# Kernel tuning notes

Hardware: AMD Instinct MI355X
Metric: run time of the kernel (lower is better)

Reference implementation:

```python
import math
import jax, jax.numpy as jnp
import numpy as np

# Model dims (from Weatherformer defaults: hidden = 8 heads * factor 8 = 64)
B, S, E, H, L = 8, 1024, 64, 8, 3
HD = E // H          # head_dim = 8
FF = 4 * E           # feedforward = 256
IN = 31              # input_dim (weather features)
OUT = 31             # output_dim
NG = 31              # granularity embedding table size
EPS = 1e-5


def setup_inputs() -> dict:
    key = jax.random.key(0)
    ks = jax.random.split(key, 12)
    p = lambda k, shape: jax.random.normal(k, shape, jnp.float32) * 0.05
    return {
        "weather": jax.random.normal(ks[0], (B, S, IN), jnp.float32),
        "coords": jax.random.uniform(ks[1], (B, 2), jnp.float32, -90.0, 90.0),
        "temporal_index": jax.random.randint(ks[2], (B, 2), 0, NG),
        "W_emb": p(ks[3], (IN, E)), "b_emb": jnp.zeros((E,), jnp.float32),
        "W_qkv": p(ks[4], (L, E, 3 * E)), "b_qkv": jnp.zeros((L, 3 * E), jnp.float32),
        "W_out": p(ks[5], (L, E, E)), "b_out": jnp.zeros((L, E), jnp.float32),
        "gran": p(ks[6], (L, NG, E)),
        "g1": jnp.ones((L, E), jnp.float32), "be1": jnp.zeros((L, E), jnp.float32),
        "W1": p(ks[7], (L, E, FF)), "b1": jnp.zeros((L, FF), jnp.float32),
        "W2": p(ks[8], (L, FF, E)), "b2": jnp.zeros((L, E), jnp.float32),
        "g2": jnp.ones((L, E), jnp.float32), "be2": jnp.zeros((L, E), jnp.float32),
        "W_fc": p(ks[9], (E, OUT)), "b_fc": jnp.zeros((OUT,), jnp.float32),
    }


def _layernorm(x, g, b):
    m = jnp.mean(x, axis=-1, keepdims=True)
    v = jnp.var(x, axis=-1, keepdims=True)
    return (x - m) / jnp.sqrt(v + EPS) * g + b


def _pos_encoding(coords):
    # div_term over every 4th channel: [E/4]
    div = jnp.exp(jnp.arange(0, E, 4, dtype=jnp.float32) * (-math.log(10000.0) / E))
    lat = coords[:, :1] / 180.0 * math.pi   # [B,1]
    lon = coords[:, 1:] / 180.0 * math.pi   # [B,1]
    tf = jnp.arange(S, dtype=jnp.float32)[:, None] * div          # [S, E/4]
    q = E // 4
    sin_tf = jnp.broadcast_to(jnp.sin(tf)[None], (B, S, q))       # channels 0::4
    cos_tf = jnp.broadcast_to(jnp.cos(tf)[None], (B, S, q))       # channels 1::4
    sin_lat = jnp.broadcast_to(jnp.sin(lat * div)[:, None, :], (B, S, q))  # 2::4
    cos_lon = jnp.broadcast_to(jnp.cos(lon * div)[:, None, :], (B, S, q))  # 3::4
    return jnp.stack([sin_tf, cos_tf, sin_lat, cos_lon], axis=-1).reshape(B, S, E)


def _attention(x, tg, W_qkv, b_qkv, W_out, b_out, gran_table):
    # Faithful replication of torch's (seq-major) qkv reshape quirk.
    qkv = x @ W_qkv + b_qkv                                  # [B,S,3E]
    qkv = qkv.reshape(B, S, 3, E).transpose(2, 0, 1, 3)      # [3,B,S,E]
    qkv = qkv.reshape(3, S, B * H, HD).transpose(0, 2, 1, 3) # [3,B*H,S,HD]
    q, k, v = qkv[0], qkv[1], qkv[2]
    ge = gran_table[tg].reshape(B * H, 1, HD)                # [B*H,1,HD]
    q = q + ge
    k = k + ge
    scores = jnp.einsum('bqd,bkd->bqk', q, k) * (HD ** -0.5) # [B*H,S,S]
    w = jax.nn.softmax(scores, axis=-1)                      # dropout = identity (eval)
    o = jnp.einsum('bqk,bkd->bqd', w, v)                     # [B*H,S,HD]
    o = o.transpose(1, 0, 2).reshape(B * S, E)
    return (o @ W_out + b_out).reshape(B, S, E)


def reference(weather, coords, temporal_index, W_emb, b_emb, W_qkv, b_qkv,
              W_out, b_out, gran, g1, be1, W1, b1, W2, b2, g2, be2, W_fc, b_fc):
    tg = temporal_index[:, 1:][:, :, None].astype(jnp.int32)  # [B,1,1]
    x = weather @ W_emb + b_emb                               # [B,S,E]
    x = x + _pos_encoding(coords)
    for l in range(L):
        a = _attention(x, tg, W_qkv[l], b_qkv[l], W_out[l], b_out[l], gran[l])
        x = _layernorm(x + a, g1[l], be1[l])
        ff = jax.nn.relu(x @ W1[l] + b1[l]) @ W2[l] + b2[l]
        x = _layernorm(x + ff, g2[l], be2[l])
    return x @ W_fc + b_fc                                    # [B,S,OUT]
```

## Files before the change

kernel.cpp:

```cpp
#include <hip/hip_runtime.h>
#include <math.h>

#define EPS 1e-5f

typedef float f32x16 __attribute__((ext_vector_type(16)));
typedef short short8 __attribute__((ext_vector_type(8)));

union U4S8 { uint4 u; short8 s; };

__device__ __forceinline__ float wave_sum64(float v) {
#pragma unroll
  for (int off = 32; off >= 1; off >>= 1) v += __shfl_xor(v, off, 64);
  return v;
}

__device__ __forceinline__ unsigned int bf16rne(float f) {
  unsigned int u = __float_as_uint(f);
  return (u + 0x7fffu + ((u >> 16) & 1u)) >> 16;
}
__device__ __forceinline__ float blo(unsigned int u) {
  return __uint_as_float(u << 16);
}
__device__ __forceinline__ float bhi(unsigned int u) {
  return __uint_as_float(u & 0xffff0000u);
}
__device__ __forceinline__ unsigned int cvt_pk_bf16(float lo, float hi) {
  unsigned int r;
  asm("v_cvt_pk_bf16_f32 %0, %1, %2" : "=v"(r) : "v"(lo), "v"(hi));
  return r;
}

__global__ __launch_bounds__(256) void k_prep(
    const float* __restrict__ Wo, const float* __restrict__ W1,
    const float* __restrict__ W2, const float* __restrict__ Wq,
    unsigned int* __restrict__ wbo, unsigned int* __restrict__ w1b,
    unsigned int* __restrict__ w2b, unsigned int* __restrict__ wqb) {
  int i = blockIdx.x * 256 + threadIdx.x;
  if (i < 6144) {
    int l = i >> 11, rem = i & 2047, p = rem >> 6, c = rem & 63;
    const float* s = Wo + l * 4096;
    wbo[i] = bf16rne(s[(2 * p) * 64 + c]) | (bf16rne(s[(2 * p + 1) * 64 + c]) << 16);
  }
  {
    int l = i / 8192, rem = i & 8191, p = rem >> 8, c = rem & 255;
    const float* s = W1 + (size_t)l * 16384;
    w1b[i] = bf16rne(s[(2 * p) * 256 + c]) | (bf16rne(s[(2 * p + 1) * 256 + c]) << 16);
  }
  {
    int l = i / 8192, rem = i & 8191, p = rem >> 6, c = rem & 63;
    const float* s = W2 + (size_t)l * 16384;
    w2b[i] = bf16rne(s[(2 * p) * 64 + c]) | (bf16rne(s[(2 * p + 1) * 64 + c]) << 16);
  }
  if (i < 12288) {
    int l = i / 6144, rem = i % 6144, p = rem / 192, c = rem % 192;
    const float* s = Wq + (size_t)(l + 1) * 12288;
    wqb[i] = bf16rne(s[(2 * p) * 192 + c]) | (bf16rne(s[(2 * p + 1) * 192 + c]) << 16);
  }
}

__global__ __launch_bounds__(192) void k_qkv0(
    const float* __restrict__ weather, const float* __restrict__ coords,
    const float* __restrict__ W_emb, const float* __restrict__ b_emb,
    const float* __restrict__ Wq, const float* __restrict__ bq,
    const float* __restrict__ gran, const int* __restrict__ tidx,
    float* __restrict__ x, unsigned int* __restrict__ qb,
    unsigned int* __restrict__ kbuf, unsigned short* __restrict__ vt) {
  int t = threadIdx.x;
  int row0 = blockIdx.x << 3;
  __shared__ float wrow[8][32];
  __shared__ float xs[8][64];
  for (int i = t; i < 256; i += 192) {
    int r = i >> 5, c2 = i & 31;
    if (c2 < 31) wrow[r][c2] = weather[(size_t)(row0 + r) * 31 + c2];
  }
  __syncthreads();
  int b = row0 >> 10;
  float lat = coords[b * 2 + 0] * 0.017453292519943295f;
  float lon = coords[b * 2 + 1] * 0.017453292519943295f;
  for (int idx = t; idx < 512; idx += 192) {
    int r = idx >> 6, e = idx & 63;
    int s = (row0 + r) & 1023;
    float acc = b_emb[e];
#pragma unroll
    for (int i = 0; i < 31; ++i) acc = fmaf(wrow[r][i], W_emb[i * 64 + e], acc);
    int g = e >> 2, rem = e & 3;
    float div = __expf(-0.5756462732485115f * (float)g);
    float pe;
    if (rem == 0)      pe = sinf((float)s * div);
    else if (rem == 1) pe = cosf((float)s * div);
    else if (rem == 2) pe = sinf(lat * div);
    else               pe = cosf(lon * div);
    float xv = acc + pe;
    xs[r][e] = xv;
    x[(size_t)(row0 + r) * 64 + e] = xv;
  }
  __syncthreads();
  float acc[8];
  float bias = bq[t];
#pragma unroll
  for (int r = 0; r < 8; ++r) acc[r] = bias;
#pragma unroll 4
  for (int k4 = 0; k4 < 16; ++k4) {
    float4 xv[8];
#pragma unroll
    for (int r = 0; r < 8; ++r) xv[r] = *(const float4*)(&xs[r][4 * k4]);
    float w0 = Wq[(4 * k4 + 0) * 192 + t];
    float w1 = Wq[(4 * k4 + 1) * 192 + t];
    float w2 = Wq[(4 * k4 + 2) * 192 + t];
    float w3 = Wq[(4 * k4 + 3) * 192 + t];
#pragma unroll
    for (int r = 0; r < 8; ++r) {
      acc[r] = fmaf(xv[r].x, w0, acc[r]);
      acc[r] = fmaf(xv[r].y, w1, acc[r]);
      acc[r] = fmaf(xv[r].z, w2, acc[r]);
      acc[r] = fmaf(xv[r].w, w3, acc[r]);
    }
  }
  int cq = t & 63;
  int hh = cq >> 3, hd = t & 7;
  int shi = (row0 & 1023) >> 3;
  int s2 = (b << 7) | shi;
  const float scl = 0.35355339059327373f;
#pragma unroll
  for (int r = 0; r < 8; ++r) {
    float o = acc[r];
    if (t < 128) o += gran[tidx[2 * r + 1] * 64 + cq];
    int bh = (r << 3) | hh;
    if (t < 64) {
      o *= scl;
      float nb = __shfl_down(o, 1, 64);
      if ((hd & 1) == 0)
        qb[((((size_t)bh << 10) | s2) << 2) + (hd >> 1)] =
            bf16rne(o) | (bf16rne(nb) << 16);
    } else if (t < 128) {
      float nb = __shfl_down(o, 1, 64);
      if ((hd & 1) == 0)
        kbuf[((((size_t)bh << 10) | s2) << 2) + (hd >> 1)] =
            bf16rne(o) | (bf16rne(nb) << 16);
    } else {
      vt[((size_t)bh << 13) + (hd << 10) + s2] = (unsigned short)bf16rne(o);
    }
  }
}

__global__ __launch_bounds__(512, 2) void k_attn(
    const unsigned int* __restrict__ qb, const unsigned int* __restrict__ kbuf,
    const unsigned short* __restrict__ vt, float* __restrict__ ao) {
  int bh = blockIdx.x >> 3, chunk = blockIdx.x & 7;
  int slo = bh >> 3, h = bh & 7;
  int t = threadIdx.x;
  int l = t & 63, w = t >> 6;
  int grp = w >> 1, kh = w & 1;
  int lq = l & 31, g = l >> 5;
  bool kl = (l < 32);
  bool vl = (lq < 8);
  int q = (chunk << 7) + (grp << 5) + lq;

  U4S8 qf;
  qf.u = make_uint4(0, 0, 0, 0);
  if (kl) qf.u = *(const uint4*)(qb + ((((size_t)bh << 10) + q) << 2));

  const uint4* kp = (const uint4*)(kbuf + ((size_t)bh << 12));
  const unsigned short* vp = vt + ((size_t)bh << 13);

  f32x16 O, Z;
#pragma unroll
  for (int i = 0; i < 16; ++i) { O[i] = 0.f; Z[i] = 0.f; }
  float m = -1e30f, ls = 0.f;

  int kb0 = kh << 4;
  for (int kblk = kb0; kblk < kb0 + 16; ++kblk) {
    U4S8 af;
    af.u = make_uint4(0, 0, 0, 0);
    if (kl) af.u = kp[(kblk << 5) + lq];
    f32x16 S = __builtin_amdgcn_mfma_f32_32x32x16_bf16(af.s, qf.s, Z, 0, 0, 0);

    float mx = S[0];
#pragma unroll
    for (int i = 1; i < 16; ++i) mx = fmaxf(mx, S[i]);
    mx = fmaxf(mx, __shfl_xor(mx, 32, 64));
    if (mx > m + 8.f) {
      float esc = __expf(m - mx);
      ls *= esc;
      O *= esc;
      m = mx;
    }
    float p[16];
#pragma unroll
    for (int i = 0; i < 16; ++i) p[i] = __expf(S[i] - m);
    float s01 = (p[0] + p[1]) + (p[2] + p[3]);
    float s23 = (p[4] + p[5]) + (p[6] + p[7]);
    float s45 = (p[8] + p[9]) + (p[10] + p[11]);
    float s67 = (p[12] + p[13]) + (p[14] + p[15]);
    ls += (s01 + s23) + (s45 + s67);

    unsigned va = cvt_pk_bf16(p[0], p[1]),  vb = cvt_pk_bf16(p[2], p[3]);
    unsigned vc = cvt_pk_bf16(p[4], p[5]),  vd = cvt_pk_bf16(p[6], p[7]);
    unsigned ve = cvt_pk_bf16(p[8], p[9]),  vf = cvt_pk_bf16(p[10], p[11]);
    unsigned vg = cvt_pk_bf16(p[12], p[13]), vh = cvt_pk_bf16(p[14], p[15]);
    unsigned sa = __shfl_xor((int)va, 32, 64), sb = __shfl_xor((int)vb, 32, 64);
    unsigned sc = __shfl_xor((int)vc, 32, 64), sd = __shfl_xor((int)vd, 32, 64);
    unsigned se = __shfl_xor((int)ve, 32, 64), sf = __shfl_xor((int)vf, 32, 64);
    unsigned sg = __shfl_xor((int)vg, 32, 64), sh = __shfl_xor((int)vh, 32, 64);
    U4S8 b1, b2;
    b1.u.x = kl ? va : sc;  b1.u.y = kl ? vb : sd;
    b1.u.z = kl ? sa : vc;  b1.u.w = kl ? sb : vd;
    b2.u.x = kl ? ve : sg;  b2.u.y = kl ? vf : sh;
    b2.u.z = kl ? se : vg;  b2.u.w = kl ? sf : vh;

    U4S8 v1, v2;
    v1.u = make_uint4(0, 0, 0, 0);
    v2.u = make_uint4(0, 0, 0, 0);
    if (vl) {
      const unsigned short* vb8 = vp + (lq << 10) + (kblk << 5) + (g << 3);
      v1.u = *(const uint4*)vb8;
      v2.u = *(const uint4*)(vb8 + 16);
    }
    O = __builtin_amdgcn_mfma_f32_32x32x16_bf16(v1.s, b1.s, O, 0, 0, 0);
    O = __builtin_amdgcn_mfma_f32_32x32x16_bf16(v2.s, b2.s, O, 0, 0, 0);
  }

  ls += __shfl_xor(ls, 32, 64);

  __shared__ float pm[4][64], pl[4][64];
  __shared__ float po[4][64][4];
  if (kh == 0) {
    pm[grp][l] = m;
    pl[grp][l] = ls;
    *(float4*)(&po[grp][l][0]) = make_float4(O[0], O[1], O[2], O[3]);
  }
  __syncthreads();
  if (kh == 1) {
    float mA = pm[grp][l], lsA = pl[grp][l];
    float nm = fmaxf(m, mA);
    float wB = __expf(m - nm), wA = __expf(mA - nm);
    float4 oA = *(const float4*)(&po[grp][l][0]);
    float inv = 1.0f / (ls * wB + lsA * wA);
    int bq2 = q >> 7, sq = ((q & 127) << 3) | slo;
    float* op = ao + (((size_t)((bq2 << 10) | sq)) << 6) + (h << 3) + (g << 2);
    *(float4*)op = make_float4((O[0] * wB + oA.x * wA) * inv,
                               (O[1] * wB + oA.y * wA) * inv,
                               (O[2] * wB + oA.z * wA) * inv,
                               (O[3] * wB + oA.w * wA) * inv);
  }
}

template <bool EMIT, bool HEAD>
__global__ __launch_bounds__(256, 4) void k_fused(
    const float* x_in, const float* __restrict__ ao,
    const unsigned int* __restrict__ Wo, const float* __restrict__ bo,
    const float* __restrict__ g1, const float* __restrict__ be1,
    const unsigned int* __restrict__ W1, const float* __restrict__ b1,
    const unsigned int* __restrict__ W2, const float* __restrict__ b2,
    const float* __restrict__ g2, const float* __restrict__ be2,
    const unsigned int* __restrict__ Wq, const float* __restrict__ bq,
    const float* __restrict__ gran, const int* __restrict__ tidx,
    unsigned int* __restrict__ qbo, unsigned int* __restrict__ kbo,
    unsigned short* __restrict__ vto,
    const float* __restrict__ Wfc, const float* __restrict__ bfc,
    float* __restrict__ outp, float* __restrict__ x_out) {
  int t = threadIdx.x, w = t >> 6, c = t & 63;
  int ws = w << 1;
  int row_base = blockIdx.x << 3;
  int row0 = row_base + ws;
  __shared__ float aos[8][64];
  __shared__ float h1s[8][256];
  float xin[2];
#pragma unroll
  for (int r = 0; r < 2; ++r) {
    aos[ws + r][c] = ao[(size_t)(row0 + r) * 64 + c];
    xin[r] = x_in[(size_t)(row0 + r) * 64 + c];
  }
  float acc[2];
  float bov = bo[c];
#pragma unroll
  for (int r = 0; r < 2; ++r) acc[r] = bov;
#pragma unroll 4
  for (int k4 = 0; k4 < 16; ++k4) {
    unsigned a = Wo[(2 * k4) * 64 + c], b = Wo[(2 * k4 + 1) * 64 + c];
    float w0 = blo(a), w1 = bhi(a), w2 = blo(b), w3 = bhi(b);
#pragma unroll
    for (int r = 0; r < 2; ++r) {
      float4 av = *(const float4*)(&aos[ws + r][4 * k4]);
      acc[r] = fmaf(av.x, w0, acc[r]);
      acc[r] = fmaf(av.y, w1, acc[r]);
      acc[r] = fmaf(av.z, w2, acc[r]);
      acc[r] = fmaf(av.w, w3, acc[r]);
    }
  }
  float g1v = g1[c], be1v = be1[c];
  float x1v[2];
#pragma unroll
  for (int r = 0; r < 2; ++r) {
    float y = acc[r] + xin[r];
    float s1 = wave_sum64(y), s2 = wave_sum64(y * y);
    float mean = s1 * 0.015625f, var = s2 * 0.015625f - mean * mean;
    x1v[r] = (y - mean) * rsqrtf(var + EPS) * g1v + be1v;
    aos[ws + r][c] = x1v[r];
  }
  float4 h[2];
  float4 b1v = *(const float4*)(b1 + 4 * c);
#pragma unroll
  for (int r = 0; r < 2; ++r) h[r] = b1v;
#pragma unroll 4
  for (int k4 = 0; k4 < 16; ++k4) {
    uint4 A = *(const uint4*)(W1 + (2 * k4) * 256 + 4 * c);
    uint4 B = *(const uint4*)(W1 + (2 * k4 + 1) * 256 + 4 * c);
    float4 w0 = make_float4(blo(A.x), blo(A.y), blo(A.z), blo(A.w));
    float4 w1 = make_float4(bhi(A.x), bhi(A.y), bhi(A.z), bhi(A.w));
    float4 w2 = make_float4(blo(B.x), blo(B.y), blo(B.z), blo(B.w));
    float4 w3 = make_float4(bhi(B.x), bhi(B.y), bhi(B.z), bhi(B.w));
#pragma unroll
    for (int r = 0; r < 2; ++r) {
      float4 xv = *(const float4*)(&aos[ws + r][4 * k4]);
      h[r].x = fmaf(xv.x, w0.x, h[r].x); h[r].y = fmaf(xv.x, w0.y, h[r].y);
      h[r].z = fmaf(xv.x, w0.z, h[r].z); h[r].w = fmaf(xv.x, w0.w, h[r].w);
      h[r].x = fmaf(xv.y, w1.x, h[r].x); h[r].y = fmaf(xv.y, w1.y, h[r].y);
      h[r].z = fmaf(xv.y, w1.z, h[r].z); h[r].w = fmaf(xv.y, w1.w, h[r].w);
      h[r].x = fmaf(xv.z, w2.x, h[r].x); h[r].y = fmaf(xv.z, w2.y, h[r].y);
      h[r].z = fmaf(xv.z, w2.z, h[r].z); h[r].w = fmaf(xv.z, w2.w, h[r].w);
      h[r].x = fmaf(xv.w, w3.x, h[r].x); h[r].y = fmaf(xv.w, w3.y, h[r].y);
      h[r].z = fmaf(xv.w, w3.z, h[r].z); h[r].w = fmaf(xv.w, w3.w, h[r].w);
    }
  }
#pragma unroll
  for (int r = 0; r < 2; ++r) {
    h[r].x = fmaxf(h[r].x, 0.f); h[r].y = fmaxf(h[r].y, 0.f);
    h[r].z = fmaxf(h[r].z, 0.f); h[r].w = fmaxf(h[r].w, 0.f);
    *(float4*)(&h1s[ws + r][4 * c]) = h[r];
  }
  float acc2[2];
  float b2v = b2[c];
#pragma unroll
  for (int r = 0; r < 2; ++r) acc2[r] = b2v;
#pragma unroll 4
  for (int k4 = 0; k4 < 64; ++k4) {
    unsigned a = W2[(2 * k4) * 64 + c], b = W2[(2 * k4 + 1) * 64 + c];
    float w0 = blo(a), w1 = bhi(a), w2 = blo(b), w3 = bhi(b);
#pragma unroll
    for (int r = 0; r < 2; ++r) {
      float4 hv = *(const float4*)(&h1s[ws + r][4 * k4]);
      acc2[r] = fmaf(hv.x, w0, acc2[r]);
      acc2[r] = fmaf(hv.y, w1, acc2[r]);
      acc2[r] = fmaf(hv.z, w2, acc2[r]);
      acc2[r] = fmaf(hv.w, w3, acc2[r]);
    }
  }
  float g2v = g2[c], be2v = be2[c];
#pragma unroll
  for (int r = 0; r < 2; ++r) {
    float y2 = acc2[r] + x1v[r];
    float t1 = wave_sum64(y2), t2 = wave_sum64(y2 * y2);
    float mean2 = t1 * 0.015625f, var2 = t2 * 0.015625f - mean2 * mean2;
    float xo = (y2 - mean2) * rsqrtf(var2 + EPS) * g2v + be2v;
    if (!HEAD) x_out[(size_t)(row0 + r) * 64 + c] = xo;
    aos[ws + r][c] = xo;
  }
  if (EMIT) {
    __syncthreads();
    if (t < 192) {
      float qa[8];
      float bias = bq[t];
#pragma unroll
      for (int r = 0; r < 8; ++r) qa[r] = bias;
#pragma unroll 4
      for (int k4 = 0; k4 < 16; ++k4) {
        unsigned a = Wq[(2 * k4) * 192 + t], b = Wq[(2 * k4 + 1) * 192 + t];
        float w0 = blo(a), w1 = bhi(a), w2v = blo(b), w3 = bhi(b);
#pragma unroll
        for (int r = 0; r < 8; ++r) {
          float4 av = *(const float4*)(&aos[r][4 * k4]);
          qa[r] = fmaf(av.x, w0, qa[r]);
          qa[r] = fmaf(av.y, w1, qa[r]);
          qa[r] = fmaf(av.z, w2v, qa[r]);
          qa[r] = fmaf(av.w, w3, qa[r]);
        }
      }
      int cq = t & 63, hh = cq >> 3, hd = t & 7;
      int bb = row_base >> 10;
      int s2 = (bb << 7) | ((row_base & 1023) >> 3);
      const float scl = 0.35355339059327373f;
#pragma unroll
      for (int r = 0; r < 8; ++r) {
        float o = qa[r];
        if (t < 128) o += gran[tidx[2 * r + 1] * 64 + cq];
        int bh = (r << 3) | hh;
        size_t base = ((size_t)(bh << 10)) | s2;
        if (t < 64) {
          o *= scl;
          float nb = __shfl_down(o, 1, 64);
          if ((hd & 1) == 0)
            qbo[(base << 2) + (hd >> 1)] = bf16rne(o) | (bf16rne(nb) << 16);
        } else if (t < 128) {
          float nb = __shfl_down(o, 1, 64);
          if ((hd & 1) == 0)
            kbo[(base << 2) + (hd >> 1)] = bf16rne(o) | (bf16rne(nb) << 16);
        } else {
          vto[((size_t)bh << 13) + (hd << 10) + s2] = (unsigned short)bf16rne(o);
        }
      }
    }
  }
  if (HEAD) {
    __syncthreads();
    int r = t >> 5, o = t & 31;
    if (o < 31) {
      float acc3 = bfc[o];
#pragma unroll 8
      for (int i = 0; i < 64; ++i)
        acc3 = fmaf(aos[r][i], Wfc[i * 31 + o], acc3);
      outp[(size_t)(row_base + r) * 31 + o] = acc3;
    }
  }
}

extern "C" void kernel_launch(void* const* d_in, const int* in_sizes, int n_in,
                              void* d_out, int out_size, void* d_ws, size_t ws_size,
                              hipStream_t stream) {
  const float* weather = (const float*)d_in[0];
  const float* coords  = (const float*)d_in[1];
  const int*   tidx    = (const int*)d_in[2];
  const float* W_emb   = (const float*)d_in[3];
  const float* b_emb   = (const float*)d_in[4];
  const float* W_qkv   = (const float*)d_in[5];
  const float* b_qkv   = (const float*)d_in[6];
  const float* W_out   = (const float*)d_in[7];
  const float* b_out   = (const float*)d_in[8];
  const float* gran    = (const float*)d_in[9];
  const float* g1      = (const float*)d_in[10];
  const float* be1     = (const float*)d_in[11];
  const float* W1      = (const float*)d_in[12];
  const float* b1      = (const float*)d_in[13];
  const float* W2      = (const float*)d_in[14];
  const float* b2      = (const float*)d_in[15];
  const float* g2      = (const float*)d_in[16];
  const float* be2     = (const float*)d_in[17];
  const float* W_fc    = (const float*)d_in[18];
  const float* b_fc    = (const float*)d_in[19];
  float* out = (float*)d_out;

  float* x = (float*)d_ws;
  unsigned int* qbw = (unsigned int*)(x + 8192 * 64);
  unsigned int* kbw = qbw + 64 * 1024 * 4;
  unsigned short* vtw = (unsigned short*)(kbw + 64 * 1024 * 4);
  float* ao = (float*)(vtw + 64 * 8 * 1024);
  unsigned int* wbo = (unsigned int*)(ao + 8192 * 64);
  unsigned int* w1b = wbo + 6144;
  unsigned int* w2b = w1b + 24576;
  unsigned int* wqb = w2b + 24576;

  k_prep<<<96, 256, 0, stream>>>(W_out, W1, W2, W_qkv, wbo, w1b, w2b, wqb);
  k_qkv0<<<1024, 192, 0, stream>>>(weather, coords, W_emb, b_emb,
                                   W_qkv, b_qkv, gran, tidx,
                                   x, qbw, kbw, vtw);
  for (int l = 0; l < 3; ++l) {
    k_attn<<<512, 512, 0, stream>>>(qbw, kbw, vtw, ao);
    if (l < 2) {
      k_fused<true, false><<<1024, 256, 0, stream>>>(
          x, ao, wbo + l * 2048, b_out + l * 64,
          g1 + l * 64, be1 + l * 64, w1b + l * 8192, b1 + l * 256,
          w2b + l * 8192, b2 + l * 64, g2 + l * 64, be2 + l * 64,
          wqb + l * 6144, b_qkv + (l + 1) * 192,
          gran + (l + 1) * 31 * 64, tidx, qbw, kbw, vtw,
          nullptr, nullptr, nullptr, x);
    } else {
      k_fused<false, true><<<1024, 256, 0, stream>>>(
          x, ao, wbo + l * 2048, b_out + l * 64,
          g1 + l * 64, be1 + l * 64, w1b + l * 8192, b1 + l * 256,
          w2b + l * 8192, b2 + l * 64, g2 + l * 64, be2 + l * 64,
          nullptr, nullptr, nullptr, nullptr, nullptr, nullptr, nullptr,
          W_fc, b_fc, out, nullptr);
    }
  }
}
```

Before: 164.9 us.

## Split attention keys four ways per query group and fold weight prep into qkv0

The attention kernel now splits the key range across four waves per query group instead of two, and each block covers 64 queries instead of 128. This doubles the grid to 1024 blocks to raise parallelism and shorten each wave's serial loop, at the cost of a four-way shared-memory softmax merge. Separately, the bf16 weight-packing kernel is removed and its work is appended to the first qkv kernel, saving one launch.

```diff
diff --git a/kernel.cpp b/kernel.cpp
--- a/kernel.cpp
+++ b/kernel.cpp
@@ -28,34 +28,6 @@
   unsigned int r;
   asm("v_cvt_pk_bf16_f32 %0, %1, %2" : "=v"(r) : "v"(lo), "v"(hi));
   return r;
-}
-
-__global__ __launch_bounds__(256) void k_prep(
-    const float* __restrict__ Wo, const float* __restrict__ W1,
-    const float* __restrict__ W2, const float* __restrict__ Wq,
-    unsigned int* __restrict__ wbo, unsigned int* __restrict__ w1b,
-    unsigned int* __restrict__ w2b, unsigned int* __restrict__ wqb) {
-  int i = blockIdx.x * 256 + threadIdx.x;
-  if (i < 6144) {
-    int l = i >> 11, rem = i & 2047, p = rem >> 6, c = rem & 63;
-    const float* s = Wo + l * 4096;
-    wbo[i] = bf16rne(s[(2 * p) * 64 + c]) | (bf16rne(s[(2 * p + 1) * 64 + c]) << 16);
-  }
-  {
-    int l = i / 8192, rem = i & 8191, p = rem >> 8, c = rem & 255;
-    const float* s = W1 + (size_t)l * 16384;
-    w1b[i] = bf16rne(s[(2 * p) * 256 + c]) | (bf16rne(s[(2 * p + 1) * 256 + c]) << 16);
-  }
-  {
-    int l = i / 8192, rem = i & 8191, p = rem >> 6, c = rem & 63;
-    const float* s = W2 + (size_t)l * 16384;
-    w2b[i] = bf16rne(s[(2 * p) * 64 + c]) | (bf16rne(s[(2 * p + 1) * 64 + c]) << 16);
-  }
-  if (i < 12288) {
-    int l = i / 6144, rem = i % 6144, p = rem / 192, c = rem % 192;
-    const float* s = Wq + (size_t)(l + 1) * 12288;
-    wqb[i] = bf16rne(s[(2 * p) * 192 + c]) | (bf16rne(s[(2 * p + 1) * 192 + c]) << 16);
-  }
 }
 
 __global__ __launch_bounds__(192) void k_qkv0(
@@ -63,8 +35,12 @@
     const float* __restrict__ W_emb, const float* __restrict__ b_emb,
     const float* __restrict__ Wq, const float* __restrict__ bq,
     const float* __restrict__ gran, const int* __restrict__ tidx,
+    const float* __restrict__ Wo_f, const float* __restrict__ W1_f,
+    const float* __restrict__ W2_f,
     float* __restrict__ x, unsigned int* __restrict__ qb,
-    unsigned int* __restrict__ kbuf, unsigned short* __restrict__ vt) {
+    unsigned int* __restrict__ kbuf, unsigned short* __restrict__ vt,
+    unsigned int* __restrict__ wbo, unsigned int* __restrict__ w1b,
+    unsigned int* __restrict__ w2b, unsigned int* __restrict__ wqb) {
   int t = threadIdx.x;
   int row0 = blockIdx.x << 3;
   __shared__ float wrow[8][32];
@@ -141,20 +117,45 @@
       vt[((size_t)bh << 13) + (hd << 10) + s2] = (unsigned short)bf16rne(o);
     }
   }
+  int gid = blockIdx.x * 192 + t;
+  if (gid < 6144) {
+    int ll = gid >> 11, rem = gid & 2047, p = rem >> 6, c2 = rem & 63;
+    const float* s = Wo_f + ll * 4096;
+    wbo[gid] = bf16rne(s[(2 * p) * 64 + c2]) |
+               (bf16rne(s[(2 * p + 1) * 64 + c2]) << 16);
+  } else if (gid < 30720) {
+    int i = gid - 6144;
+    int ll = i / 8192, rem = i & 8191, p = rem >> 8, c2 = rem & 255;
+    const float* s = W1_f + (size_t)ll * 16384;
+    w1b[i] = bf16rne(s[(2 * p) * 256 + c2]) |
+             (bf16rne(s[(2 * p + 1) * 256 + c2]) << 16);
+  } else if (gid < 55296) {
+    int i = gid - 30720;
+    int ll = i / 8192, rem = i & 8191, p = rem >> 6, c2 = rem & 63;
+    const float* s = W2_f + (size_t)ll * 16384;
+    w2b[i] = bf16rne(s[(2 * p) * 64 + c2]) |
+             (bf16rne(s[(2 * p + 1) * 64 + c2]) << 16);
+  } else if (gid < 67584) {
+    int i = gid - 55296;
+    int ll = i / 6144, rem = i % 6144, p = rem / 192, c2 = rem % 192;
+    const float* s = Wq + (size_t)(ll + 1) * 12288;
+    wqb[i] = bf16rne(s[(2 * p) * 192 + c2]) |
+             (bf16rne(s[(2 * p + 1) * 192 + c2]) << 16);
+  }
 }
 
 __global__ __launch_bounds__(512, 2) void k_attn(
     const unsigned int* __restrict__ qb, const unsigned int* __restrict__ kbuf,
     const unsigned short* __restrict__ vt, float* __restrict__ ao) {
-  int bh = blockIdx.x >> 3, chunk = blockIdx.x & 7;
+  int bh = blockIdx.x >> 4, chunk = blockIdx.x & 15;
   int slo = bh >> 3, h = bh & 7;
   int t = threadIdx.x;
   int l = t & 63, w = t >> 6;
-  int grp = w >> 1, kh = w & 1;
+  int grp = w >> 2, kh = w & 3;
   int lq = l & 31, g = l >> 5;
   bool kl = (l < 32);
   bool vl = (lq < 8);
-  int q = (chunk << 7) + (grp << 5) + lq;
+  int q = (chunk << 6) + (grp << 5) + lq;
 
   U4S8 qf;
   qf.u = make_uint4(0, 0, 0, 0);
@@ -168,8 +169,8 @@
   for (int i = 0; i < 16; ++i) { O[i] = 0.f; Z[i] = 0.f; }
   float m = -1e30f, ls = 0.f;
 
-  int kb0 = kh << 4;
-  for (int kblk = kb0; kblk < kb0 + 16; ++kblk) {
+  int kb0 = kh << 3;
+  for (int kblk = kb0; kblk < kb0 + 8; ++kblk) {
     U4S8 af;
     af.u = make_uint4(0, 0, 0, 0);
     if (kl) af.u = kp[(kblk << 5) + lq];
@@ -222,26 +223,33 @@
 
   ls += __shfl_xor(ls, 32, 64);
 
-  __shared__ float pm[4][64], pl[4][64];
-  __shared__ float po[4][64][4];
+  __shared__ float pm[2][4][64], pl[2][4][64];
+  __shared__ float po[2][4][64][4];
+  pm[grp][kh][l] = m;
+  pl[grp][kh][l] = ls;
+  *(float4*)(&po[grp][kh][l][0]) = make_float4(O[0], O[1], O[2], O[3]);
+  __syncthreads();
   if (kh == 0) {
-    pm[grp][l] = m;
-    pl[grp][l] = ls;
-    *(float4*)(&po[grp][l][0]) = make_float4(O[0], O[1], O[2], O[3]);
-  }
-  __syncthreads();
-  if (kh == 1) {
-    float mA = pm[grp][l], lsA = pl[grp][l];
-    float nm = fmaxf(m, mA);
-    float wB = __expf(m - nm), wA = __expf(mA - nm);
-    float4 oA = *(const float4*)(&po[grp][l][0]);
-    float inv = 1.0f / (ls * wB + lsA * wA);
+    float M = m;
+#pragma unroll
+    for (int j = 1; j < 4; ++j) M = fmaxf(M, pm[grp][j][l]);
+    float w0 = __expf(m - M);
+    float L = ls * w0;
+    float o0 = O[0] * w0, o1 = O[1] * w0, o2 = O[2] * w0, o3 = O[3] * w0;
+#pragma unroll
+    for (int j = 1; j < 4; ++j) {
+      float wj = __expf(pm[grp][j][l] - M);
+      L = fmaf(pl[grp][j][l], wj, L);
+      float4 oj = *(const float4*)(&po[grp][j][l][0]);
+      o0 = fmaf(oj.x, wj, o0);
+      o1 = fmaf(oj.y, wj, o1);
+      o2 = fmaf(oj.z, wj, o2);
+      o3 = fmaf(oj.w, wj, o3);
+    }
+    float inv = 1.0f / L;
     int bq2 = q >> 7, sq = ((q & 127) << 3) | slo;
     float* op = ao + (((size_t)((bq2 << 10) | sq)) << 6) + (h << 3) + (g << 2);
-    *(float4*)op = make_float4((O[0] * wB + oA.x * wA) * inv,
-                               (O[1] * wB + oA.y * wA) * inv,
-                               (O[2] * wB + oA.z * wA) * inv,
-                               (O[3] * wB + oA.w * wA) * inv);
+    *(float4*)op = make_float4(o0 * inv, o1 * inv, o2 * inv, o3 * inv);
   }
 }
 
@@ -449,12 +457,12 @@
   unsigned int* w2b = w1b + 24576;
   unsigned int* wqb = w2b + 24576;
 
-  k_prep<<<96, 256, 0, stream>>>(W_out, W1, W2, W_qkv, wbo, w1b, w2b, wqb);
   k_qkv0<<<1024, 192, 0, stream>>>(weather, coords, W_emb, b_emb,
                                    W_qkv, b_qkv, gran, tidx,
-                                   x, qbw, kbw, vtw);
+                                   W_out, W1, W2,
+                                   x, qbw, kbw, vtw, wbo, w1b, w2b, wqb);
   for (int l = 0; l < 3; ++l) {
-    k_attn<<<512, 512, 0, stream>>>(qbw, kbw, vtw, ao);
+    k_attn<<<1024, 512, 0, stream>>>(qbw, kbw, vtw, ao);
     if (l < 2) {
       k_fused<true, false><<<1024, 256, 0, stream>>>(
           x, ao, wbo + l * 2048, b_out + l * 64,
```

New measurement: 156.9 us (median of 2 runs). 1.05x faster.
